# Optimization experiments

Hardware: AMD Instinct MI355X
Metric: run time of the kernel (lower is better)

Reference implementation:

```python
import jax, jax.numpy as jnp
import numpy as np

B, T, C, H = 2, 2048, 1024, 16
HD = C // H  # head_dim = 64


def setup_inputs() -> dict:
    key = jax.random.key(0)
    ks = jax.random.split(key, 5)
    x = jax.random.normal(ks[0], (B, T, C), dtype=jnp.float32)
    # realistic rotary tables: cos/sin of position*inv_freq, shape (T, HD//2)
    inv_freq = 1.0 / (10000.0 ** (jnp.arange(0, HD, 2, dtype=jnp.float32) / HD))
    ang = jnp.arange(T, dtype=jnp.float32)[:, None] * inv_freq[None, :]
    cos, sin = jnp.cos(ang), jnp.sin(ang)
    w_attn = jax.random.normal(ks[1], (C, 3 * C), dtype=jnp.float32) * (C ** -0.5)
    b_attn = jnp.zeros((3 * C,), dtype=jnp.float32)
    w_proj = jax.random.normal(ks[2], (C, C), dtype=jnp.float32) * (C ** -0.5)
    b_proj = jnp.zeros((C,), dtype=jnp.float32)
    return {"x": x, "cos": cos, "sin": sin, "w_attn": w_attn, "b_attn": b_attn,
            "w_proj": w_proj, "b_proj": b_proj}


def _apply_rotary(x, cos, sin):
    # x: (B, H, T, HD); cos/sin: (T, HD//2) broadcast over B,H
    x_even = x[..., ::2]
    x_odd = x[..., 1::2]
    rot = jnp.stack((x_even * cos - x_odd * sin, x_even * sin + x_odd * cos), axis=-1)
    return rot.reshape(*x.shape[:-1], x.shape[-1])


def reference(x, cos, sin, w_attn, b_attn, w_proj, b_proj):
    b, t, c = x.shape
    qkv = x @ w_attn + b_attn                       # (B, T, 3C)
    q, k, v = jnp.split(qkv, 3, axis=-1)
    # (B, T, C) -> (B, H, T, HD)
    def to_heads(z):
        return z.reshape(b, t, H, HD).transpose(0, 2, 1, 3)
    q, k, v = to_heads(q), to_heads(k), to_heads(v)
    q = _apply_rotary(q, cos, sin)
    k = _apply_rotary(k, cos, sin)
    scale = 1.0 / jnp.sqrt(jnp.asarray(HD, dtype=x.dtype))
    scores = jnp.einsum('bhqd,bhkd->bhqk', q, k) * scale
    causal = jnp.tril(jnp.ones((t, t), dtype=bool))
    scores = jnp.where(causal, scores, jnp.asarray(-jnp.inf, dtype=scores.dtype))
    attn = jax.nn.softmax(scores, axis=-1)
    y = jnp.einsum('bhqk,bhkd->bhqd', attn, v)      # (B, H, T, HD)
    y = y.transpose(0, 2, 1, 3).reshape(b, t, c)
    return y @ w_proj + b_proj
```

## Files before the change

kernel.cpp:

```cpp
#include <hip/hip_runtime.h>
#include <hip/hip_bf16.h>
#include <math.h>

#define Bsz 2
#define Tseq 2048
#define Cdim 1024
#define Hn 16
#define HDim 64
#define Mrows 4096
#define N3 3072
#define QSCALE 0.1803368801111137f

typedef __bf16 bf16_t;
typedef __bf16 bf16x4 __attribute__((ext_vector_type(4)));
typedef __bf16 bf16x8 __attribute__((ext_vector_type(8)));
typedef float floatx4 __attribute__((ext_vector_type(4)));

__device__ __forceinline__ void async16(const void* g, void* l) {
    __builtin_amdgcn_global_load_lds(
        (const __attribute__((address_space(1))) void*)g,
        (__attribute__((address_space(3))) void*)l, 16, 0, 0);
}

__global__ __launch_bounds__(256) void prep_kernel(
    const float* __restrict__ x, const float* __restrict__ w_attn,
    const float* __restrict__ w_proj, bf16_t* __restrict__ xb,
    bf16_t* __restrict__ waT, bf16_t* __restrict__ wpT)
{
    __shared__ float Ts[32][33];
    const int bid = blockIdx.x;
    if (bid < 2048) {
        size_t g = (size_t)bid * 256 + threadIdx.x;
        float4 a = *(const float4*)(x + g * 8);
        float4 b = *(const float4*)(x + g * 8 + 4);
        bf16x8 o;
        o[0] = (bf16_t)a.x; o[1] = (bf16_t)a.y; o[2] = (bf16_t)a.z; o[3] = (bf16_t)a.w;
        o[4] = (bf16_t)b.x; o[5] = (bf16_t)b.y; o[6] = (bf16_t)b.z; o[7] = (bf16_t)b.w;
        *(bf16x8*)(xb + g * 8) = o;
        return;
    }
    const float* in; bf16_t* out; int R, C, bx, by;
    if (bid < 5120) {
        int t = bid - 2048; in = w_attn; out = waT; R = Cdim; C = N3;
        bx = t % 96; by = t / 96;
    } else {
        int t = bid - 5120; in = w_proj; out = wpT; R = Cdim; C = Cdim;
        bx = t & 31; by = t >> 5;
    }
    int c0 = bx << 5, r0 = by << 5;
    int lr = threadIdx.x >> 3, lc = (threadIdx.x & 7) << 2;
    float4 v = *(const float4*)(in + (size_t)(r0 + lr) * C + c0 + lc);
    Ts[lr][lc] = v.x; Ts[lr][lc + 1] = v.y; Ts[lr][lc + 2] = v.z; Ts[lr][lc + 3] = v.w;
    __syncthreads();
    bf16x4 o;
    o[0] = (bf16_t)Ts[lc + 0][lr]; o[1] = (bf16_t)Ts[lc + 1][lr];
    o[2] = (bf16_t)Ts[lc + 2][lr]; o[3] = (bf16_t)Ts[lc + 3][lr];
    *(bf16x4*)(out + (size_t)(c0 + lr) * R + r0 + lc) = o;
}

__global__ __launch_bounds__(256) void gemm_qkv(
    const bf16_t* __restrict__ xb, const bf16_t* __restrict__ waT,
    const float* __restrict__ bias, const float* __restrict__ cosb,
    const float* __restrict__ sinb,
    bf16_t* __restrict__ qb, bf16_t* __restrict__ kb, bf16_t* __restrict__ vt)
{
    __shared__ bf16_t As[128 * 32];
    __shared__ bf16_t Bs[128 * 32];
    const int tid = threadIdx.x;
    const int lane = tid & 63, w = tid >> 6;
    const int lm = lane & 15, quad = lane >> 4;
    const int wy = w >> 1, wx = w & 1;
    const int m0 = blockIdx.y << 7, n0 = blockIdx.x << 7;

    const floatx4 fz = {0.f, 0.f, 0.f, 0.f};
    floatx4 acc[4][4];
    #pragma unroll
    for (int i = 0; i < 4; i++)
        #pragma unroll
        for (int j = 0; j < 4; j++) acc[i][j] = fz;

    const bf16_t* Ag = xb + (size_t)m0 * Cdim;
    const bf16_t* Bg = waT + (size_t)n0 * Cdim;

    for (int k0 = 0; k0 < Cdim; k0 += 32) {
        #pragma unroll
        for (int it = 0; it < 2; ++it) {
            int ci = (w << 7) + (it << 6) + lane;
            int row = ci >> 2, cq = (ci & 3) ^ (row & 3);
            async16(Ag + (size_t)row * Cdim + k0 + cq * 8, As + ((w << 7) + (it << 6)) * 8);
            async16(Bg + (size_t)row * Cdim + k0 + cq * 8, Bs + ((w << 7) + (it << 6)) * 8);
        }
        __syncthreads();
        bf16x8 af[4], bfr[4];
        #pragma unroll
        for (int i = 0; i < 4; i++) {
            int row = (wy << 6) + (i << 4) + lm;
            int cq = quad ^ (lm & 3);
            af[i] = *(const bf16x8*)&As[row * 32 + cq * 8];
        }
        #pragma unroll
        for (int j = 0; j < 4; j++) {
            int row = (wx << 6) + (j << 4) + lm;
            int cq = quad ^ (lm & 3);
            bfr[j] = *(const bf16x8*)&Bs[row * 32 + cq * 8];
        }
        #pragma unroll
        for (int i = 0; i < 4; i++)
            #pragma unroll
            for (int j = 0; j < 4; j++)
                acc[i][j] = __builtin_amdgcn_mfma_f32_16x16x32_bf16(af[i], bfr[j], acc[i][j], 0, 0, 0);
        __syncthreads();
    }

    const int sec = n0 >> 10;
    const int mb = m0 + (wy << 6);
    const int nb = n0 + (wx << 6);
    #pragma unroll
    for (int i = 0; i < 4; i++) {
        int mrow0 = mb + (i << 4) + (quad << 2);
        int b = mrow0 >> 11, t0 = mrow0 & 2047;
        #pragma unroll
        for (int j = 0; j < 4; j++) {
            int n = nb + (j << 4) + lm;
            float bi = bias[n];
            int rel = n & 1023;
            int h = rel >> 6, hd = rel & 63;
            if (sec == 2) {
                int tp = (t0 & ~31) | (((t0 >> 2) & 3) << 3) | (((t0 >> 4) & 1) << 2);
                bf16x4 pk;
                #pragma unroll
                for (int r = 0; r < 4; r++) pk[r] = (bf16_t)(acc[i][j][r] + bi);
                *(bf16x4*)&vt[((size_t)(b * Hn + h) * HDim + hd) * Tseq + tp] = pk;
            } else {
                bf16_t* dst = (sec == 0) ? qb : kb;
                const int ih = hd >> 1;
                const bool ev = !(hd & 1);
                #pragma unroll
                for (int r = 0; r < 4; r++) {
                    int t = t0 + r;
                    float v = acc[i][j][r] + bi;
                    float x = __shfl_xor(v, 1);
                    float c = cosb[t * 32 + ih], s = sinb[t * 32 + ih];
                    float rv = ev ? (v * c - x * s) : (x * s + v * c);
                    if (sec == 0) rv *= QSCALE;
                    dst[((size_t)(b * Hn + h) * Tseq + t) * HDim + hd] = (bf16_t)rv;
                }
            }
        }
    }
}

__global__ __launch_bounds__(256) void attn_mfma(
    const bf16_t* __restrict__ qb, const bf16_t* __restrict__ kb,
    const bf16_t* __restrict__ vt, bf16_t* __restrict__ yb)
{
    __shared__ bf16_t Ks[2][64 * 64];
    __shared__ bf16_t VTs[2][64 * 64];

    const int pp = blockIdx.x & 15;
    const int bh = blockIdx.x >> 4;
    const int b = bh >> 4, h = bh & 15;
    const int tid = threadIdx.x;
    const int w4 = tid >> 6, lane = tid & 63, lm = lane & 15, quad = lane >> 4;
    const int jt0 = pp, jt1 = 31 - pp;
    const int nk = 32 - pp;

    {
        const bf16_t* Kg = kb + (size_t)bh * Tseq * HDim;
        const bf16_t* Vg = vt + (size_t)bh * HDim * Tseq;
        #pragma unroll
        for (int it = 0; it < 2; ++it) {
            int ci = (it << 8) + tid;
            int row = ci >> 3, cq = (ci & 7) ^ (row & 7);
            async16(Kg + row * HDim + cq * 8, &Ks[0][((it << 8) + (w4 << 6)) * 8]);
            async16(Vg + (size_t)row * Tseq + cq * 8, &VTs[0][((it << 8) + (w4 << 6)) * 8]);
        }
    }

    bf16x8 qf[2][2];
    #pragma unroll
    for (int t = 0; t < 2; ++t) {
        int qrow = ((t ? jt1 : jt0) << 6) + (w4 << 4) + lm;
        const bf16_t* Qg = qb + ((size_t)bh * Tseq + qrow) * HDim;
        #pragma unroll
        for (int ks = 0; ks < 2; ++ks)
            qf[t][ks] = *(const bf16x8*)(Qg + (ks << 5) + (quad << 3));
    }
    __syncthreads();

    const floatx4 fz = {0.f, 0.f, 0.f, 0.f};
    floatx4 o_[2][4];
    #pragma unroll
    for (int t = 0; t < 2; ++t)
        #pragma unroll
        for (int f = 0; f < 4; ++f) o_[t][f] = fz;
    float l_[2] = {0.f, 0.f};
    const int lastk[2] = {pp, 31 - pp};
    const int qq[2] = {(jt0 << 6) + (w4 << 4) + lm, (jt1 << 6) + (w4 << 4) + lm};

    for (int kt = 0; kt < nk; ++kt) {
        const int cb = kt & 1;
        if (kt + 1 < nk) {
            const int nb2 = cb ^ 1;
            const bf16_t* Kg = kb + ((size_t)bh * Tseq + ((kt + 1) << 6)) * HDim;
            const bf16_t* Vg = vt + (size_t)bh * HDim * Tseq + ((kt + 1) << 6);
            #pragma unroll
            for (int it = 0; it < 2; ++it) {
                int ci = (it << 8) + tid;
                int row = ci >> 3, cq = (ci & 7) ^ (row & 7);
                async16(Kg + row * HDim + cq * 8, &Ks[nb2][((it << 8) + (w4 << 6)) * 8]);
                async16(Vg + (size_t)row * Tseq + cq * 8, &VTs[nb2][((it << 8) + (w4 << 6)) * 8]);
            }
        }

        floatx4 st[2][4];
        #pragma unroll
        for (int t = 0; t < 2; ++t)
            #pragma unroll
            for (int sub = 0; sub < 4; ++sub) st[t][sub] = fz;
        #pragma unroll
        for (int ks = 0; ks < 2; ++ks) {
            bf16x8 kf[4];
            #pragma unroll
            for (int sub = 0; sub < 4; ++sub) {
                int krow = (sub << 4) + lm;
                int kc = ((ks << 2) + quad) ^ (krow & 7);
                kf[sub] = *(const bf16x8*)&Ks[cb][krow * 64 + kc * 8];
            }
            if (kt <= lastk[0])
                #pragma unroll
                for (int sub = 0; sub < 4; ++sub)
                    st[0][sub] = __builtin_amdgcn_mfma_f32_16x16x32_bf16(
                        kf[sub], qf[0][ks], st[0][sub], 0, 0, 0);
            #pragma unroll
            for (int sub = 0; sub < 4; ++sub)
                st[1][sub] = __builtin_amdgcn_mfma_f32_16x16x32_bf16(
                    kf[sub], qf[1][ks], st[1][sub], 0, 0, 0);
        }

        bf16x8 pf[2][2];
        #pragma unroll
        for (int t = 0; t < 2; ++t) {
            if (kt > lastk[t]) continue;
            const bool dm = (kt == lastk[t]);
            float rs = 0.f;
            #pragma unroll
            for (int cc = 0; cc < 2; ++cc)
                #pragma unroll
                for (int jj = 0; jj < 8; ++jj) {
                    int sub = (cc << 1) + (jj >> 2), r = jj & 3;
                    float val = st[t][sub][r];
                    if (dm) {
                        int key = (kt << 6) + (sub << 4) + (quad << 2) + r;
                        if (key > qq[t]) val = -3e38f;
                    }
                    float p = exp2f(val);
                    rs += p;
                    pf[t][cc][jj] = (bf16_t)p;
                }
            rs += __shfl_xor(rs, 16);
            rs += __shfl_xor(rs, 32);
            l_[t] += rs;
        }

        #pragma unroll
        for (int cc = 0; cc < 2; ++cc) {
            bf16x8 vf[4];
            #pragma unroll
            for (int f = 0; f < 4; ++f) {
                int vrow = (f << 4) + lm;
                int vc = ((cc << 2) + quad) ^ (vrow & 7);
                vf[f] = *(const bf16x8*)&VTs[cb][vrow * 64 + vc * 8];
            }
            #pragma unroll
            for (int t = 0; t < 2; ++t) {
                if (kt > lastk[t]) continue;
                #pragma unroll
                for (int f = 0; f < 4; ++f)
                    o_[t][f] = __builtin_amdgcn_mfma_f32_16x16x32_bf16(
                        vf[f], pf[t][cc], o_[t][f], 0, 0, 0);
            }
        }
        __syncthreads();
    }

    #pragma unroll
    for (int t = 0; t < 2; ++t) {
        float inv = 1.f / l_[t];
        size_t base = ((size_t)(b * Tseq) + qq[t]) * Cdim + (h << 6) + (quad << 2);
        #pragma unroll
        for (int f = 0; f < 4; ++f) {
            bf16x4 ov;
            #pragma unroll
            for (int r = 0; r < 4; ++r) ov[r] = (bf16_t)(o_[t][f][r] * inv);
            *(bf16x4*)&yb[base + (f << 4)] = ov;
        }
    }
}

__global__ __launch_bounds__(256) void gemm_proj(
    const bf16_t* __restrict__ yb, const bf16_t* __restrict__ wpT,
    const float* __restrict__ bias, float* __restrict__ out)
{
    __shared__ bf16_t As[128 * 32];
    __shared__ bf16_t Bs[128 * 32];
    const int tid = threadIdx.x;
    const int lane = tid & 63, w = tid >> 6;
    const int lm = lane & 15, quad = lane >> 4;
    const int wy = w >> 1, wx = w & 1;
    const int m0 = blockIdx.y << 7, n0 = blockIdx.x << 7;

    const floatx4 fz = {0.f, 0.f, 0.f, 0.f};
    floatx4 acc[4][4];
    #pragma unroll
    for (int i = 0; i < 4; i++)
        #pragma unroll
        for (int j = 0; j < 4; j++) acc[i][j] = fz;

    const bf16_t* Ag = yb + (size_t)m0 * Cdim;
    const bf16_t* Bg = wpT + (size_t)n0 * Cdim;

    for (int k0 = 0; k0 < Cdim; k0 += 32) {
        #pragma unroll
        for (int it = 0; it < 2; ++it) {
            int ci = (w << 7) + (it << 6) + lane;
            int row = ci >> 2, cq = (ci & 3) ^ (row & 3);
            async16(Ag + (size_t)row * Cdim + k0 + cq * 8, As + ((w << 7) + (it << 6)) * 8);
            async16(Bg + (size_t)row * Cdim + k0 + cq * 8, Bs + ((w << 7) + (it << 6)) * 8);
        }
        __syncthreads();
        bf16x8 af[4], bfr[4];
        #pragma unroll
        for (int i = 0; i < 4; i++) {
            int row = (wy << 6) + (i << 4) + lm;
            int cq = quad ^ (lm & 3);
            af[i] = *(const bf16x8*)&As[row * 32 + cq * 8];
        }
        #pragma unroll
        for (int j = 0; j < 4; j++) {
            int row = (wx << 6) + (j << 4) + lm;
            int cq = quad ^ (lm & 3);
            bfr[j] = *(const bf16x8*)&Bs[row * 32 + cq * 8];
        }
        #pragma unroll
        for (int i = 0; i < 4; i++)
            #pragma unroll
            for (int j = 0; j < 4; j++)
                acc[i][j] = __builtin_amdgcn_mfma_f32_16x16x32_bf16(af[i], bfr[j], acc[i][j], 0, 0, 0);
        __syncthreads();
    }

    const int mb = m0 + (wy << 6);
    const int nb = n0 + (wx << 6);
    #pragma unroll
    for (int i = 0; i < 4; i++) {
        int mrow0 = mb + (i << 4) + (quad << 2);
        #pragma unroll
        for (int j = 0; j < 4; j++) {
            int n = nb + (j << 4) + lm;
            float bi = bias[n];
            #pragma unroll
            for (int r = 0; r < 4; r++)
                out[(size_t)(mrow0 + r) * Cdim + n] = acc[i][j][r] + bi;
        }
    }
}

extern "C" void kernel_launch(void* const* d_in, const int* in_sizes, int n_in,
                              void* d_out, int out_size, void* d_ws, size_t ws_size,
                              hipStream_t stream) {
    const float* x      = (const float*)d_in[0];
    const float* cosb   = (const float*)d_in[1];
    const float* sinb   = (const float*)d_in[2];
    const float* w_attn = (const float*)d_in[3];
    const float* b_attn = (const float*)d_in[4];
    const float* w_proj = (const float*)d_in[5];
    const float* b_proj = (const float*)d_in[6];

    char* ws = (char*)d_ws;
    bf16_t* xb  = (bf16_t*)(ws);
    bf16_t* waT = (bf16_t*)(ws + (size_t)(8 << 20));
    bf16_t* wpT = (bf16_t*)(ws + (size_t)(14 << 20));
    bf16_t* qb  = (bf16_t*)(ws + (size_t)(16 << 20));
    bf16_t* kb  = (bf16_t*)(ws + (size_t)(24 << 20));
    bf16_t* vtb = (bf16_t*)(ws + (size_t)(32 << 20));
    bf16_t* yb  = (bf16_t*)(ws + (size_t)(40 << 20));

    prep_kernel<<<6144, 256, 0, stream>>>(x, w_attn, w_proj, xb, waT, wpT);
    gemm_qkv<<<dim3(24, 32), 256, 0, stream>>>(xb, waT, b_attn, cosb, sinb, qb, kb, vtb);
    attn_mfma<<<512, 256, 0, stream>>>(qb, kb, vtb, yb);
    gemm_proj<<<dim3(8, 32), 256, 0, stream>>>(yb, wpT, b_proj, (float*)d_out);
}
```

Before: 204.4 us.

## Widen GEMM K-step to 64 and split attention into one query tile per block

Both GEMM kernels now load a 64-wide K slice per iteration with an 8-way XOR swizzle, so the main loop syncs half as often and issues more MFMAs per barrier. The attention kernel drops the paired-query-tile scheme, where each block handled tiles pp and 31-pp to balance causal work. It now launches a 32x32 grid with one 64-row query tile per block, ordered from longest to shortest. This doubles the number of blocks and lowers register pressure, but gives up the built-in load balancing and K/V reuse across the two tiles, leaving block scheduling to handle the uneven work.

```diff
diff --git a/kernel.cpp b/kernel.cpp
--- a/kernel.cpp
+++ b/kernel.cpp
@@ -64,8 +64,8 @@
     const float* __restrict__ sinb,
     bf16_t* __restrict__ qb, bf16_t* __restrict__ kb, bf16_t* __restrict__ vt)
 {
-    __shared__ bf16_t As[128 * 32];
-    __shared__ bf16_t Bs[128 * 32];
+    __shared__ bf16_t As[128 * 64];
+    __shared__ bf16_t Bs[128 * 64];
     const int tid = threadIdx.x;
     const int lane = tid & 63, w = tid >> 6;
     const int lm = lane & 15, quad = lane >> 4;
@@ -82,33 +82,39 @@
     const bf16_t* Ag = xb + (size_t)m0 * Cdim;
     const bf16_t* Bg = waT + (size_t)n0 * Cdim;
 
-    for (int k0 = 0; k0 < Cdim; k0 += 32) {
-        #pragma unroll
-        for (int it = 0; it < 2; ++it) {
-            int ci = (w << 7) + (it << 6) + lane;
-            int row = ci >> 2, cq = (ci & 3) ^ (row & 3);
-            async16(Ag + (size_t)row * Cdim + k0 + cq * 8, As + ((w << 7) + (it << 6)) * 8);
-            async16(Bg + (size_t)row * Cdim + k0 + cq * 8, Bs + ((w << 7) + (it << 6)) * 8);
-        }
-        __syncthreads();
-        bf16x8 af[4], bfr[4];
-        #pragma unroll
-        for (int i = 0; i < 4; i++) {
-            int row = (wy << 6) + (i << 4) + lm;
-            int cq = quad ^ (lm & 3);
-            af[i] = *(const bf16x8*)&As[row * 32 + cq * 8];
-        }
-        #pragma unroll
-        for (int j = 0; j < 4; j++) {
-            int row = (wx << 6) + (j << 4) + lm;
-            int cq = quad ^ (lm & 3);
-            bfr[j] = *(const bf16x8*)&Bs[row * 32 + cq * 8];
-        }
-        #pragma unroll
-        for (int i = 0; i < 4; i++)
-            #pragma unroll
-            for (int j = 0; j < 4; j++)
-                acc[i][j] = __builtin_amdgcn_mfma_f32_16x16x32_bf16(af[i], bfr[j], acc[i][j], 0, 0, 0);
+    for (int k0 = 0; k0 < Cdim; k0 += 64) {
+        #pragma unroll
+        for (int it = 0; it < 4; ++it) {
+            int ci = (it << 8) + tid;
+            int row = ci >> 3, cq = (ci & 7) ^ (row & 7);
+            async16(Ag + (size_t)row * Cdim + k0 + cq * 8,
+                    As + (size_t)((it << 8) + (w << 6)) * 8);
+            async16(Bg + (size_t)row * Cdim + k0 + cq * 8,
+                    Bs + (size_t)((it << 8) + (w << 6)) * 8);
+        }
+        __syncthreads();
+        #pragma unroll
+        for (int ks = 0; ks < 2; ++ks) {
+            bf16x8 af[4], bfr[4];
+            #pragma unroll
+            for (int i = 0; i < 4; i++) {
+                int row = (wy << 6) + (i << 4) + lm;
+                int ph = ((ks << 2) + quad) ^ (row & 7);
+                af[i] = *(const bf16x8*)&As[row * 64 + ph * 8];
+            }
+            #pragma unroll
+            for (int j = 0; j < 4; j++) {
+                int row = (wx << 6) + (j << 4) + lm;
+                int ph = ((ks << 2) + quad) ^ (row & 7);
+                bfr[j] = *(const bf16x8*)&Bs[row * 64 + ph * 8];
+            }
+            #pragma unroll
+            for (int i = 0; i < 4; i++)
+                #pragma unroll
+                for (int j = 0; j < 4; j++)
+                    acc[i][j] = __builtin_amdgcn_mfma_f32_16x16x32_bf16(
+                        af[i], bfr[j], acc[i][j], 0, 0, 0);
+        }
         __syncthreads();
     }
 
@@ -157,13 +163,12 @@
     __shared__ bf16_t Ks[2][64 * 64];
     __shared__ bf16_t VTs[2][64 * 64];
 
-    const int pp = blockIdx.x & 15;
-    const int bh = blockIdx.x >> 4;
+    const int qt = 31 - blockIdx.x;
+    const int bh = blockIdx.y;
     const int b = bh >> 4, h = bh & 15;
     const int tid = threadIdx.x;
     const int w4 = tid >> 6, lane = tid & 63, lm = lane & 15, quad = lane >> 4;
-    const int jt0 = pp, jt1 = 31 - pp;
-    const int nk = 32 - pp;
+    const int nk = qt + 1;
 
     {
         const bf16_t* Kg = kb + (size_t)bh * Tseq * HDim;
@@ -177,26 +182,21 @@
         }
     }
 
-    bf16x8 qf[2][2];
-    #pragma unroll
-    for (int t = 0; t < 2; ++t) {
-        int qrow = ((t ? jt1 : jt0) << 6) + (w4 << 4) + lm;
-        const bf16_t* Qg = qb + ((size_t)bh * Tseq + qrow) * HDim;
+    const int qq = (qt << 6) + (w4 << 4) + lm;
+    bf16x8 qf[2];
+    {
+        const bf16_t* Qg = qb + ((size_t)bh * Tseq + qq) * HDim;
         #pragma unroll
         for (int ks = 0; ks < 2; ++ks)
-            qf[t][ks] = *(const bf16x8*)(Qg + (ks << 5) + (quad << 3));
+            qf[ks] = *(const bf16x8*)(Qg + (ks << 5) + (quad << 3));
     }
     __syncthreads();
 
     const floatx4 fz = {0.f, 0.f, 0.f, 0.f};
-    floatx4 o_[2][4];
-    #pragma unroll
-    for (int t = 0; t < 2; ++t)
-        #pragma unroll
-        for (int f = 0; f < 4; ++f) o_[t][f] = fz;
-    float l_[2] = {0.f, 0.f};
-    const int lastk[2] = {pp, 31 - pp};
-    const int qq[2] = {(jt0 << 6) + (w4 << 4) + lm, (jt1 << 6) + (w4 << 4) + lm};
+    floatx4 o_[4];
+    #pragma unroll
+    for (int f = 0; f < 4; ++f) o_[f] = fz;
+    float l_ = 0.f;
 
     for (int kt = 0; kt < nk; ++kt) {
         const int cb = kt & 1;
@@ -213,11 +213,9 @@
             }
         }
 
-        floatx4 st[2][4];
-        #pragma unroll
-        for (int t = 0; t < 2; ++t)
-            #pragma unroll
-            for (int sub = 0; sub < 4; ++sub) st[t][sub] = fz;
+        floatx4 st[4];
+        #pragma unroll
+        for (int sub = 0; sub < 4; ++sub) st[sub] = fz;
         #pragma unroll
         for (int ks = 0; ks < 2; ++ks) {
             bf16x8 kf[4];
@@ -227,40 +225,33 @@
                 int kc = ((ks << 2) + quad) ^ (krow & 7);
                 kf[sub] = *(const bf16x8*)&Ks[cb][krow * 64 + kc * 8];
             }
-            if (kt <= lastk[0])
-                #pragma unroll
-                for (int sub = 0; sub < 4; ++sub)
-                    st[0][sub] = __builtin_amdgcn_mfma_f32_16x16x32_bf16(
-                        kf[sub], qf[0][ks], st[0][sub], 0, 0, 0);
             #pragma unroll
             for (int sub = 0; sub < 4; ++sub)
-                st[1][sub] = __builtin_amdgcn_mfma_f32_16x16x32_bf16(
-                    kf[sub], qf[1][ks], st[1][sub], 0, 0, 0);
-        }
-
-        bf16x8 pf[2][2];
-        #pragma unroll
-        for (int t = 0; t < 2; ++t) {
-            if (kt > lastk[t]) continue;
-            const bool dm = (kt == lastk[t]);
+                st[sub] = __builtin_amdgcn_mfma_f32_16x16x32_bf16(
+                    kf[sub], qf[ks], st[sub], 0, 0, 0);
+        }
+
+        bf16x8 pf[2];
+        {
+            const bool dm = (kt == qt);
             float rs = 0.f;
             #pragma unroll
             for (int cc = 0; cc < 2; ++cc)
                 #pragma unroll
                 for (int jj = 0; jj < 8; ++jj) {
                     int sub = (cc << 1) + (jj >> 2), r = jj & 3;
-                    float val = st[t][sub][r];
+                    float val = st[sub][r];
                     if (dm) {
                         int key = (kt << 6) + (sub << 4) + (quad << 2) + r;
-                        if (key > qq[t]) val = -3e38f;
+                        if (key > qq) val = -3e38f;
                     }
                     float p = exp2f(val);
                     rs += p;
-                    pf[t][cc][jj] = (bf16_t)p;
+                    pf[cc][jj] = (bf16_t)p;
                 }
             rs += __shfl_xor(rs, 16);
             rs += __shfl_xor(rs, 32);
-            l_[t] += rs;
+            l_ += rs;
         }
 
         #pragma unroll
@@ -273,26 +264,21 @@
                 vf[f] = *(const bf16x8*)&VTs[cb][vrow * 64 + vc * 8];
             }
             #pragma unroll
-            for (int t = 0; t < 2; ++t) {
-                if (kt > lastk[t]) continue;
-                #pragma unroll
-                for (int f = 0; f < 4; ++f)
-                    o_[t][f] = __builtin_amdgcn_mfma_f32_16x16x32_bf16(
-                        vf[f], pf[t][cc], o_[t][f], 0, 0, 0);
-            }
-        }
-        __syncthreads();
-    }
-
-    #pragma unroll
-    for (int t = 0; t < 2; ++t) {
-        float inv = 1.f / l_[t];
-        size_t base = ((size_t)(b * Tseq) + qq[t]) * Cdim + (h << 6) + (quad << 2);
+            for (int f = 0; f < 4; ++f)
+                o_[f] = __builtin_amdgcn_mfma_f32_16x16x32_bf16(
+                    vf[f], pf[cc], o_[f], 0, 0, 0);
+        }
+        __syncthreads();
+    }
+
+    {
+        float inv = 1.f / l_;
+        size_t base = ((size_t)(b * Tseq) + qq) * Cdim + (h << 6) + (quad << 2);
         #pragma unroll
         for (int f = 0; f < 4; ++f) {
             bf16x4 ov;
             #pragma unroll
-            for (int r = 0; r < 4; ++r) ov[r] = (bf16_t)(o_[t][f][r] * inv);
+            for (int r = 0; r < 4; ++r) ov[r] = (bf16_t)(o_[f][r] * inv);
             *(bf16x4*)&yb[base + (f << 4)] = ov;
         }
     }
@@ -302,8 +288,8 @@
     const bf16_t* __restrict__ yb, const bf16_t* __restrict__ wpT,
     const float* __restrict__ bias, float* __restrict__ out)
 {
-    __shared__ bf16_t As[128 * 32];
-    __shared__ bf16_t Bs[128 * 32];
+    __shared__ bf16_t As[128 * 64];
+    __shared__ bf16_t Bs[128 * 64];
     const int tid = threadIdx.x;
     const int lane = tid & 63, w = tid >> 6;
     const int lm = lane & 15, quad = lane >> 4;
@@ -320,33 +306,39 @@
     const bf16_t* Ag = yb + (size_t)m0 * Cdim;
     const bf16_t* Bg = wpT + (size_t)n0 * Cdim;
 
-    for (int k0 = 0; k0 < Cdim; k0 += 32) {
-        #pragma unroll
-        for (int it = 0; it < 2; ++it) {
-            int ci = (w << 7) + (it << 6) + lane;
-            int row = ci >> 2, cq = (ci & 3) ^ (row & 3);
-            async16(Ag + (size_t)row * Cdim + k0 + cq * 8, As + ((w << 7) + (it << 6)) * 8);
-            async16(Bg + (size_t)row * Cdim + k0 + cq * 8, Bs + ((w << 7) + (it << 6)) * 8);
-        }
-        __syncthreads();
-        bf16x8 af[4], bfr[4];
-        #pragma unroll
-        for (int i = 0; i < 4; i++) {
-            int row = (wy << 6) + (i << 4) + lm;
-            int cq = quad ^ (lm & 3);
-            af[i] = *(const bf16x8*)&As[row * 32 + cq * 8];
-        }
-        #pragma unroll
-        for (int j = 0; j < 4; j++) {
-            int row = (wx << 6) + (j << 4) + lm;
-            int cq = quad ^ (lm & 3);
-            bfr[j] = *(const bf16x8*)&Bs[row * 32 + cq * 8];
-        }
-        #pragma unroll
-        for (int i = 0; i < 4; i++)
-            #pragma unroll
-            for (int j = 0; j < 4; j++)
-                acc[i][j] = __builtin_amdgcn_mfma_f32_16x16x32_bf16(af[i], bfr[j], acc[i][j], 0, 0, 0);
+    for (int k0 = 0; k0 < Cdim; k0 += 64) {
+        #pragma unroll
+        for (int it = 0; it < 4; ++it) {
+            int ci = (it << 8) + tid;
+            int row = ci >> 3, cq = (ci & 7) ^ (row & 7);
+            async16(Ag + (size_t)row * Cdim + k0 + cq * 8,
+                    As + (size_t)((it << 8) + (w << 6)) * 8);
+            async16(Bg + (size_t)row * Cdim + k0 + cq * 8,
+                    Bs + (size_t)((it << 8) + (w << 6)) * 8);
+        }
+        __syncthreads();
+        #pragma unroll
+        for (int ks = 0; ks < 2; ++ks) {
+            bf16x8 af[4], bfr[4];
+            #pragma unroll
+            for (int i = 0; i < 4; i++) {
+                int row = (wy << 6) + (i << 4) + lm;
+                int ph = ((ks << 2) + quad) ^ (row & 7);
+                af[i] = *(const bf16x8*)&As[row * 64 + ph * 8];
+            }
+            #pragma unroll
+            for (int j = 0; j < 4; j++) {
+                int row = (wx << 6) + (j << 4) + lm;
+                int ph = ((ks << 2) + quad) ^ (row & 7);
+                bfr[j] = *(const bf16x8*)&Bs[row * 64 + ph * 8];
+            }
+            #pragma unroll
+            for (int i = 0; i < 4; i++)
+                #pragma unroll
+                for (int j = 0; j < 4; j++)
+                    acc[i][j] = __builtin_amdgcn_mfma_f32_16x16x32_bf16(
+                        af[i], bfr[j], acc[i][j], 0, 0, 0);
+        }
         __syncthreads();
     }
 
@@ -388,6 +380,6 @@
 
     prep_kernel<<<6144, 256, 0, stream>>>(x, w_attn, w_proj, xb, waT, wpT);
     gemm_qkv<<<dim3(24, 32), 256, 0, stream>>>(xb, waT, b_attn, cosb, sinb, qb, kb, vtb);
-    attn_mfma<<<512, 256, 0, stream>>>(qb, kb, vtb, yb);
+    attn_mfma<<<dim3(32, 32), 256, 0, stream>>>(qb, kb, vtb, yb);
     gemm_proj<<<dim3(8, 32), 256, 0, stream>>>(yb, wpT, b_proj, (float*)d_out);
 }
```

After: 223.7 us. 1.09x slower.

## Split attention KV loop across two blocks with partial-sum reduce kernel

Applied to the files above, without the earlier changes.

Each attention block is split into two blocks that handle the even and odd key tiles respectively, doubling the grid from 512 to 1024 blocks for better CU occupancy on the MI355X. Unnormalized partial outputs and row sums are written to workspace, and a new reduce kernel adds them, normalizes, and writes y in (B,T,C) layout. The softmax appears to use a fixed max, since only l is combined and no max is rescaled, so the split is exact under that scheme. The cost is an extra kernel launch, extra global traffic for the partials, and bf16 rounding of the unnormalized partials.

```diff
diff --git a/kernel.cpp b/kernel.cpp
--- a/kernel.cpp
+++ b/kernel.cpp
@@ -152,22 +152,26 @@
 
 __global__ __launch_bounds__(256) void attn_mfma(
     const bf16_t* __restrict__ qb, const bf16_t* __restrict__ kb,
-    const bf16_t* __restrict__ vt, bf16_t* __restrict__ yb)
+    const bf16_t* __restrict__ vt, bf16_t* __restrict__ op0,
+    bf16_t* __restrict__ op1, float* __restrict__ lp0, float* __restrict__ lp1)
 {
     __shared__ bf16_t Ks[2][64 * 64];
     __shared__ bf16_t VTs[2][64 * 64];
 
-    const int pp = blockIdx.x & 15;
-    const int bh = blockIdx.x >> 4;
-    const int b = bh >> 4, h = bh & 15;
+    const int pp = blockIdx.x >> 1;
+    const int ck = blockIdx.x & 1;
+    const int bh = blockIdx.y;
     const int tid = threadIdx.x;
     const int w4 = tid >> 6, lane = tid & 63, lm = lane & 15, quad = lane >> 4;
     const int jt0 = pp, jt1 = 31 - pp;
     const int nk = 32 - pp;
 
+    bf16_t* opart = ck ? op1 : op0;
+    float* lpart = ck ? lp1 : lp0;
+
     {
-        const bf16_t* Kg = kb + (size_t)bh * Tseq * HDim;
-        const bf16_t* Vg = vt + (size_t)bh * HDim * Tseq;
+        const bf16_t* Kg = kb + ((size_t)bh * Tseq + (ck << 6)) * HDim;
+        const bf16_t* Vg = vt + (size_t)bh * HDim * Tseq + (ck << 6);
         #pragma unroll
         for (int it = 0; it < 2; ++it) {
             int ci = (it << 8) + tid;
@@ -198,12 +202,12 @@
     const int lastk[2] = {pp, 31 - pp};
     const int qq[2] = {(jt0 << 6) + (w4 << 4) + lm, (jt1 << 6) + (w4 << 4) + lm};
 
-    for (int kt = 0; kt < nk; ++kt) {
-        const int cb = kt & 1;
-        if (kt + 1 < nk) {
+    for (int kt = ck; kt < nk; kt += 2) {
+        const int cb = (kt >> 1) & 1;
+        if (kt + 2 < nk) {
             const int nb2 = cb ^ 1;
-            const bf16_t* Kg = kb + ((size_t)bh * Tseq + ((kt + 1) << 6)) * HDim;
-            const bf16_t* Vg = vt + (size_t)bh * HDim * Tseq + ((kt + 1) << 6);
+            const bf16_t* Kg = kb + ((size_t)bh * Tseq + ((kt + 2) << 6)) * HDim;
+            const bf16_t* Vg = vt + (size_t)bh * HDim * Tseq + ((kt + 2) << 6);
             #pragma unroll
             for (int it = 0; it < 2; ++it) {
                 int ci = (it << 8) + tid;
@@ -286,15 +290,40 @@
 
     #pragma unroll
     for (int t = 0; t < 2; ++t) {
-        float inv = 1.f / l_[t];
-        size_t base = ((size_t)(b * Tseq) + qq[t]) * Cdim + (h << 6) + (quad << 2);
+        size_t row_id = (size_t)bh * Tseq + qq[t];
+        size_t base = row_id * 64 + (quad << 2);
         #pragma unroll
         for (int f = 0; f < 4; ++f) {
             bf16x4 ov;
             #pragma unroll
-            for (int r = 0; r < 4; ++r) ov[r] = (bf16_t)(o_[t][f][r] * inv);
-            *(bf16x4*)&yb[base + (f << 4)] = ov;
-        }
+            for (int r = 0; r < 4; ++r) ov[r] = (bf16_t)o_[t][f][r];
+            *(bf16x4*)&opart[base + (f << 4)] = ov;
+        }
+        if (quad == 0) lpart[row_id] = l_[t];
+    }
+}
+
+__global__ __launch_bounds__(256) void reduce_kernel(
+    const bf16_t* __restrict__ op0, const bf16_t* __restrict__ op1,
+    const float* __restrict__ lp0, const float* __restrict__ lp1,
+    bf16_t* __restrict__ yb)
+{
+    int r = blockIdx.x * 256 + threadIdx.x;
+    int bh = r >> 11, q = r & 2047;
+    int b = bh >> 4, h = bh & 15;
+    float inv = 1.f / (lp0[r] + lp1[r]);
+    const bf16_t* a = op0 + (size_t)r * 64;
+    const bf16_t* c = op1 + (size_t)r * 64;
+    bf16_t* dst = yb + ((size_t)(b * Tseq + q)) * Cdim + (h << 6);
+    #pragma unroll
+    for (int v = 0; v < 8; ++v) {
+        bf16x8 x0 = *(const bf16x8*)(a + v * 8);
+        bf16x8 x1 = *(const bf16x8*)(c + v * 8);
+        bf16x8 o;
+        #pragma unroll
+        for (int e = 0; e < 8; ++e)
+            o[e] = (bf16_t)(((float)x0[e] + (float)x1[e]) * inv);
+        *(bf16x8*)(dst + v * 8) = o;
     }
 }
 
@@ -385,9 +414,14 @@
     bf16_t* kb  = (bf16_t*)(ws + (size_t)(24 << 20));
     bf16_t* vtb = (bf16_t*)(ws + (size_t)(32 << 20));
     bf16_t* yb  = (bf16_t*)(ws + (size_t)(40 << 20));
+    bf16_t* op0 = (bf16_t*)(ws);
+    bf16_t* op1 = (bf16_t*)(ws + (size_t)(48 << 20));
+    float*  lp0 = (float*)(ws + (size_t)(56 << 20));
+    float*  lp1 = (float*)(ws + (size_t)(56 << 20) + 262144);
 
     prep_kernel<<<6144, 256, 0, stream>>>(x, w_attn, w_proj, xb, waT, wpT);
     gemm_qkv<<<dim3(24, 32), 256, 0, stream>>>(xb, waT, b_attn, cosb, sinb, qb, kb, vtb);
-    attn_mfma<<<512, 256, 0, stream>>>(qb, kb, vtb, yb);
+    attn_mfma<<<dim3(32, 32), 256, 0, stream>>>(qb, kb, vtb, op0, op1, lp0, lp1);
+    reduce_kernel<<<256, 256, 0, stream>>>(op0, op1, lp0, lp1, yb);
     gemm_proj<<<dim3(8, 32), 256, 0, stream>>>(yb, wpT, b_proj, (float*)d_out);
 }
```

Result: slower. 213.6 us (+4.5%).
